# Optimization experiments

Measured on AMD Instinct MI355X. Metric: run time of the kernel, lower is better.

The kernel has to match this reference:

```python
import jax, jax.numpy as jnp
import numpy as np

D = 2048
H = 16
HD = D // H
EPS = 1e-5

def setup_inputs() -> dict:
    key = jax.random.key(0)
    ks = jax.random.split(key, 7)
    B, S = 4, 2048
    scale = 1.0 / np.sqrt(D)
    return {
        "hidden_states": jax.random.normal(ks[0], (B, S, D), dtype=jnp.float32),
        "ln_gamma": jnp.ones((D,), dtype=jnp.float32),
        "ln_beta": jnp.zeros((D,), dtype=jnp.float32),
        "W_qkv": jax.random.normal(ks[1], (D, 3 * D), dtype=jnp.float32) * scale,
        "b_qkv": jnp.zeros((3 * D,), dtype=jnp.float32),
        "W_proj": jax.random.normal(ks[2], (D, D), dtype=jnp.float32) * scale,
        "b_proj": jnp.zeros((D,), dtype=jnp.float32),
    }

def reference(hidden_states, ln_gamma, ln_beta, W_qkv, b_qkv, W_proj, b_proj):
    B, S, _ = hidden_states.shape
    # LayerNorm (fused into QKV projection in the original kernel)
    mu = jnp.mean(hidden_states, axis=-1, keepdims=True)
    var = jnp.mean(jnp.square(hidden_states - mu), axis=-1, keepdims=True)
    x = (hidden_states - mu) * jax.lax.rsqrt(var + EPS) * ln_gamma + ln_beta
    # QKV projection
    qkv = jnp.einsum("bsd,de->bse", x, W_qkv) + b_qkv  # [B,S,3D]
    q, k, v = jnp.split(qkv, 3, axis=-1)
    # split heads -> [B,H,S,hd]
    q = q.reshape(B, S, H, HD).transpose(0, 2, 1, 3)
    k = k.reshape(B, S, H, HD).transpose(0, 2, 1, 3)
    v = v.reshape(B, S, H, HD).transpose(0, 2, 1, 3)
    # scaled causal attention
    scores = jnp.einsum("bhqd,bhkd->bhqk", q, k) / jnp.asarray(np.sqrt(HD), q.dtype)
    causal = jnp.tril(jnp.ones((S, S), dtype=bool))
    neg = jnp.finfo(scores.dtype).min
    scores = jnp.where(causal, scores, neg)
    attn = jax.nn.softmax(scores, axis=-1)
    out = jnp.einsum("bhqk,bhkd->bhqd", attn, v)
    # merge heads, output projection (dropout is identity in eval / p=0)
    out = out.transpose(0, 2, 1, 3).reshape(B, S, D)
    return jnp.einsum("bsd,de->bse", out, W_proj) + b_proj
```

## Files before the change

### kernel.cpp

```cpp
#include <hip/hip_runtime.h>
#include <cstdint>

typedef __attribute__((ext_vector_type(8))) short bf16x8;
typedef __attribute__((ext_vector_type(4))) float f32x4;
typedef unsigned short u16;
typedef unsigned int u32;

constexpr int D   = 2048;
constexpr int H   = 16;
constexpr int HD  = 128;
constexpr int BATCH = 4;
constexpr int S   = 2048;
constexpr int ROWS = BATCH * S;
constexpr int N3D = 3 * D;
constexpr int QKW = 2 * D;

__device__ __forceinline__ u16 f2bf(float f) {
    union { float f; u32 u; } v; v.f = f;
    u32 r = v.u + 0x7FFFu + ((v.u >> 16) & 1u);
    return (u16)(r >> 16);
}

__device__ __forceinline__ void gld_lds16(const u16* g, u16* l) {
    __builtin_amdgcn_global_load_lds(
        (const __attribute__((address_space(1))) void*)g,
        (__attribute__((address_space(3))) void*)l, 16, 0, 0);
}

__global__ __launch_bounds__(256) void ln_bf16_kernel(
    const float* __restrict__ x, const float* __restrict__ gamma,
    const float* __restrict__ beta, u16* __restrict__ out)
{
    const int row = blockIdx.x;
    const int t = threadIdx.x;
    const float* xr = x + (size_t)row * D;
    float4 a = ((const float4*)xr)[2*t];
    float4 b = ((const float4*)xr)[2*t+1];
    float s  = a.x+a.y+a.z+a.w + b.x+b.y+b.z+b.w;
    float ss = a.x*a.x+a.y*a.y+a.z*a.z+a.w*a.w + b.x*b.x+b.y*b.y+b.z*b.z+b.w*b.w;
    #pragma unroll
    for (int off = 32; off > 0; off >>= 1) {
        s  += __shfl_down(s, off);
        ss += __shfl_down(ss, off);
    }
    __shared__ float red[8];
    const int wave = t >> 6, lane = t & 63;
    if (lane == 0) { red[wave] = s; red[4+wave] = ss; }
    __syncthreads();
    const float mu   = (red[0]+red[1]+red[2]+red[3]) * (1.0f/D);
    const float var  = (red[4]+red[5]+red[6]+red[7]) * (1.0f/D) - mu*mu;
    const float rstd = rsqrtf(var + 1e-5f);
    float4 g0  = ((const float4*)gamma)[2*t];
    float4 g1  = ((const float4*)gamma)[2*t+1];
    float4 be0 = ((const float4*)beta)[2*t];
    float4 be1 = ((const float4*)beta)[2*t+1];
    union { uint4 v; u16 e[8]; } o;
    o.e[0] = f2bf((a.x-mu)*rstd*g0.x + be0.x);
    o.e[1] = f2bf((a.y-mu)*rstd*g0.y + be0.y);
    o.e[2] = f2bf((a.z-mu)*rstd*g0.z + be0.z);
    o.e[3] = f2bf((a.w-mu)*rstd*g0.w + be0.w);
    o.e[4] = f2bf((b.x-mu)*rstd*g1.x + be1.x);
    o.e[5] = f2bf((b.y-mu)*rstd*g1.y + be1.y);
    o.e[6] = f2bf((b.z-mu)*rstd*g1.z + be1.z);
    o.e[7] = f2bf((b.w-mu)*rstd*g1.w + be1.w);
    ((uint4*)(out + (size_t)row*D))[t] = o.v;
}

__global__ __launch_bounds__(256) void transpose_bf16_kernel(
    const float* __restrict__ in, u16* __restrict__ out, int K, int N)
{
    __shared__ u16 tile[64][65];
    const int tn0 = blockIdx.x * 64;
    const int tk0 = blockIdx.y * 64;
    const int t = threadIdx.x;
    const int tx = t & 63;
    const int ty = t >> 6;
    #pragma unroll
    for (int i = 0; i < 16; i++) {
        int k = ty + i*4;
        tile[k][tx] = f2bf(in[(size_t)(tk0+k)*N + tn0 + tx]);
    }
    __syncthreads();
    #pragma unroll
    for (int i = 0; i < 16; i++) {
        int n = ty + i*4;
        out[(size_t)(tn0+n)*K + tk0 + tx] = tile[tx][n];
    }
}

constexpr int BM = 128, BN = 128, BK = 32;

template<int MODE>
__global__ __launch_bounds__(256) void gemm_bt_kernel(
    const u16* __restrict__ A, const u16* __restrict__ Bt,
    const float* __restrict__ bias, void* __restrict__ Cout,
    u16* __restrict__ vtb, int M, int N, int K)
{
    __shared__ u16 sA[BM * BK];
    __shared__ u16 sB[BN * BK];
    const int t = threadIdx.x;
    const int wave = t >> 6, lane = t & 63;
    const int lr = lane & 15, lq = lane >> 4;
    const int wm = (wave >> 1) * 64, wn = (wave & 1) * 64;
    const int m0 = blockIdx.y * BM, n0 = blockIdx.x * BN;

    const int srow = wave * 32 + (lane >> 2);
    const int scb  = (lane & 3) ^ ((lane >> 3) & 3);
    const int scol = scb * 8;
    u16* ldsA0 = sA + (wave*2 + 0) * 512;
    u16* ldsA1 = sA + (wave*2 + 1) * 512;
    u16* ldsB0 = sB + (wave*2 + 0) * 512;
    u16* ldsB1 = sB + (wave*2 + 1) * 512;
    const u16* gA0 = A  + (size_t)(m0 + srow     ) * K + scol;
    const u16* gA1 = A  + (size_t)(m0 + srow + 16) * K + scol;
    const u16* gB0 = Bt + (size_t)(n0 + srow     ) * K + scol;
    const u16* gB1 = Bt + (size_t)(n0 + srow + 16) * K + scol;

    const int rblk = (lq ^ ((lr >> 1) & 3)) * 8;

    f32x4 acc[4][4];
    #pragma unroll
    for (int i = 0; i < 4; i++)
        #pragma unroll
        for (int j = 0; j < 4; j++)
            acc[i][j] = (f32x4)(0.0f);

    for (int k0 = 0; k0 < K; k0 += BK) {
        __syncthreads();
        gld_lds16(gA0 + k0, ldsA0);
        gld_lds16(gA1 + k0, ldsA1);
        gld_lds16(gB0 + k0, ldsB0);
        gld_lds16(gB1 + k0, ldsB1);
        __syncthreads();
        bf16x8 af[4], bfr[4];
        #pragma unroll
        for (int mt = 0; mt < 4; mt++)
            af[mt] = *(const bf16x8*)(sA + (wm + mt*16 + lr) * BK + rblk);
        #pragma unroll
        for (int nt = 0; nt < 4; nt++)
            bfr[nt] = *(const bf16x8*)(sB + (wn + nt*16 + lr) * BK + rblk);
        #pragma unroll
        for (int mt = 0; mt < 4; mt++)
            #pragma unroll
            for (int nt = 0; nt < 4; nt++)
                acc[mt][nt] = __builtin_amdgcn_mfma_f32_16x16x32_bf16(
                    af[mt], bfr[nt], acc[mt][nt], 0, 0, 0);
    }

    #pragma unroll
    for (int mt = 0; mt < 4; mt++) {
        #pragma unroll
        for (int nt = 0; nt < 4; nt++) {
            const int col = n0 + wn + nt*16 + lr;
            const float bv = bias[col];
            const int row0 = m0 + wm + mt*16 + lq*4;
            float v[4];
            #pragma unroll
            for (int r = 0; r < 4; r++) v[r] = acc[mt][nt][r] + bv;
            if (MODE == 0) {
                #pragma unroll
                for (int r = 0; r < 4; r++)
                    ((float*)Cout)[(size_t)(row0 + r) * N + col] = v[r];
            } else {
                if (n0 < QKW) {
                    #pragma unroll
                    for (int r = 0; r < 4; r++)
                        ((u16*)Cout)[(size_t)(row0 + r) * QKW + col] = f2bf(v[r]);
                } else {
                    const int vcol = col - QKW;
                    const int b = row0 >> 11, s0 = row0 & 2047;
                    ushort4 pk;
                    pk.x = f2bf(v[0]); pk.y = f2bf(v[1]);
                    pk.z = f2bf(v[2]); pk.w = f2bf(v[3]);
                    *(ushort4*)(vtb + ((size_t)(b*H + (vcol >> 7)) * HD
                                       + (vcol & 127)) * S + s0) = pk;
                }
            }
        }
    }
}

constexpr int TQ = 64, TK = 64;
constexpr int KPAD = 136;
constexpr int VPAD = 72;
constexpr int PPAD = 72;

__global__ __launch_bounds__(256) void attn_kernel(
    const u16* __restrict__ qkb, const u16* __restrict__ vtb,
    u16* __restrict__ ctx)
{
    __shared__ u16 sK[TK * KPAD];
    __shared__ u16 sVT[HD * VPAD];
    __shared__ u16 sP[4 * 16 * PPAD];

    const int flat = blockIdx.x;
    const int qt = 31 - (flat >> 6);
    const int bh = flat & 63;
    const int b  = bh >> 4, h = bh & 15;
    const int q0 = qt * TQ;
    const int t = threadIdx.x;
    const int wave = t >> 6, lane = t & 63;
    const int lr = lane & 15, lq = lane >> 4;

    const u16* baseQK = qkb + (size_t)b * S * QKW + h * HD;
    const u16* baseVT = vtb + (size_t)bh * HD * S;

    const int qrow = q0 + wave * 16 + lr;
    bf16x8 qf[4];
    #pragma unroll
    for (int kc = 0; kc < 4; kc++)
        qf[kc] = *(const bf16x8*)(baseQK + (size_t)qrow * QKW + kc*32 + lq*8);

    float m_r[4], l_r[4];
    f32x4 o[8];
    #pragma unroll
    for (int r = 0; r < 4; r++) { m_r[r] = -1e30f; l_r[r] = 0.0f; }
    #pragma unroll
    for (int j = 0; j < 8; j++) o[j] = (f32x4)(0.0f);

    const float scale = 0.08838834764831845f;
    const int nkt = qt + 1;

    for (int kt = 0; kt < nkt; kt++) {
        __syncthreads();
        #pragma unroll
        for (int i = 0; i < 4; i++) {
            int c = t + i * 256;
            int krow = c >> 4, kcol = (c & 15) * 8;
            uint4 v = *(const uint4*)(baseQK + D + (size_t)(kt*TK + krow) * QKW + kcol);
            *(uint4*)(sK + krow * KPAD + kcol) = v;
        }
        #pragma unroll
        for (int i = 0; i < 4; i++) {
            int c = t + i * 256;
            int vrow = c >> 3, coff = (c & 7) * 8;
            uint4 v = *(const uint4*)(baseVT + (size_t)vrow * S + kt*TK + coff);
            *(uint4*)(sVT + vrow * VPAD + coff) = v;
        }
        __syncthreads();

        f32x4 sc[4];
        #pragma unroll
        for (int nt = 0; nt < 4; nt++) sc[nt] = (f32x4)(0.0f);
        #pragma unroll
        for (int nt = 0; nt < 4; nt++)
            #pragma unroll
            for (int kc = 0; kc < 4; kc++) {
                bf16x8 kf = *(const bf16x8*)(sK + (nt*16 + lr) * KPAD + kc*32 + lq*8);
                sc[nt] = __builtin_amdgcn_mfma_f32_16x16x32_bf16(qf[kc], kf, sc[nt], 0, 0, 0);
            }

        const bool diag = (kt == qt);
        float rowmax[4] = {-1e30f, -1e30f, -1e30f, -1e30f};
        const int qgb = q0 + wave*16 + lq*4;
        #pragma unroll
        for (int nt = 0; nt < 4; nt++)
            #pragma unroll
            for (int r = 0; r < 4; r++) {
                float sv = sc[nt][r] * scale;
                if (diag) {
                    const int kg = kt*TK + nt*16 + lr;
                    if (kg > qgb + r) sv = -1e30f;
                }
                sc[nt][r] = sv;
                rowmax[r] = fmaxf(rowmax[r], sv);
            }
        #pragma unroll
        for (int mask = 1; mask < 16; mask <<= 1)
            #pragma unroll
            for (int r = 0; r < 4; r++)
                rowmax[r] = fmaxf(rowmax[r], __shfl_xor(rowmax[r], mask));

        float alpha[4];
        #pragma unroll
        for (int r = 0; r < 4; r++) {
            float nm = fmaxf(m_r[r], rowmax[r]);
            alpha[r] = __expf(m_r[r] - nm);
            m_r[r] = nm;
        }

        u16* pw = sP + wave * 16 * PPAD;
        #pragma unroll
        for (int nt = 0; nt < 4; nt++) {
            #pragma unroll
            for (int r = 0; r < 4; r++) {
                float p = __expf(sc[nt][r] - m_r[r]);
                sc[nt][r] = p;
                pw[(lq*4 + r) * PPAD + nt*16 + lr] = f2bf(p);
            }
        }
        #pragma unroll
        for (int r = 0; r < 4; r++) {
            float psum = sc[0][r] + sc[1][r] + sc[2][r] + sc[3][r];
            l_r[r] = l_r[r] * alpha[r] + psum;
        }
        #pragma unroll
        for (int j = 0; j < 8; j++)
            #pragma unroll
            for (int r = 0; r < 4; r++)
                o[j][r] *= alpha[r];

        #pragma unroll
        for (int kc2 = 0; kc2 < 2; kc2++) {
            bf16x8 pa = *(const bf16x8*)(pw + lr * PPAD + kc2*32 + lq*8);
            #pragma unroll
            for (int n2 = 0; n2 < 8; n2++) {
                bf16x8 vb = *(const bf16x8*)(sVT + (n2*16 + lr) * VPAD + kc2*32 + lq*8);
                o[n2] = __builtin_amdgcn_mfma_f32_16x16x32_bf16(pa, vb, o[n2], 0, 0, 0);
            }
        }
    }

    #pragma unroll
    for (int mask = 1; mask < 16; mask <<= 1)
        #pragma unroll
        for (int r = 0; r < 4; r++)
            l_r[r] += __shfl_xor(l_r[r], mask);
    float inv_l[4];
    #pragma unroll
    for (int r = 0; r < 4; r++) inv_l[r] = 1.0f / l_r[r];
    #pragma unroll
    for (int n2 = 0; n2 < 8; n2++)
        #pragma unroll
        for (int r = 0; r < 4; r++) {
            const int qg = q0 + wave*16 + lq*4 + r;
            const float v = o[n2][r] * inv_l[r];
            ctx[(size_t)(b * S + qg) * D + h * HD + n2*16 + lr] = f2bf(v);
        }
}

extern "C" void kernel_launch(void* const* d_in, const int* in_sizes, int n_in,
                              void* d_out, int out_size, void* d_ws, size_t ws_size,
                              hipStream_t stream) {
    const float* hs    = (const float*)d_in[0];
    const float* gamma = (const float*)d_in[1];
    const float* beta  = (const float*)d_in[2];
    const float* Wqkv  = (const float*)d_in[3];
    const float* bqkv  = (const float*)d_in[4];
    const float* Wproj = (const float*)d_in[5];
    const float* bproj = (const float*)d_in[6];

    char* ws = (char*)d_ws;
    size_t off = 0;
    u16* xb   = (u16*)(ws + off); off += (size_t)ROWS * D * 2;
    u16* wtq  = (u16*)(ws + off); off += (size_t)N3D * D * 2;
    u16* wtp  = (u16*)(ws + off); off += (size_t)D * D * 2;
    u16* qkb  = (u16*)(ws + off); off += (size_t)ROWS * QKW * 2;
    u16* vtb  = (u16*)(ws + off); off += (size_t)ROWS * D * 2;
    u16* ctxb = (u16*)(ws + off);

    ln_bf16_kernel<<<ROWS, 256, 0, stream>>>(hs, gamma, beta, xb);
    transpose_bf16_kernel<<<dim3(N3D/64, D/64), 256, 0, stream>>>(Wqkv, wtq, D, N3D);
    transpose_bf16_kernel<<<dim3(D/64,   D/64), 256, 0, stream>>>(Wproj, wtp, D, D);
    gemm_bt_kernel<2><<<dim3(N3D/BN, ROWS/BM), 256, 0, stream>>>(
        xb, wtq, bqkv, qkb, vtb, ROWS, N3D, D);
    attn_kernel<<<dim3((S/TQ) * BATCH * H), 256, 0, stream>>>(qkb, vtb, ctxb);
    gemm_bt_kernel<0><<<dim3(D/BN, ROWS/BM), 256, 0, stream>>>(
        ctxb, wtp, bproj, (float*)d_out, nullptr, ROWS, D, D);
}
```

Before: 698.3 us.

## Use 256x256 GEMM tiles with 4-stage async LDS prefetch pipeline

Replaces the 128x128 single-buffered GEMM with a 256x256 tile, 512-thread kernel that keeps a 4-slot ring of LDS buffers filled by direct global-to-LDS loads issued three k-steps ahead. Waiting on partial vmcnt lets loads overlap the MFMA work, and setprio raises the wave's priority around the MFMA bursts. The LDS XOR swizzle is dropped, which may bring back bank conflicts. The larger tiles give fewer blocks, which may hurt occupancy and load balance, especially for the smaller output projection.

```diff
diff --git a/kernel.cpp b/kernel.cpp
--- a/kernel.cpp
+++ b/kernel.cpp
@@ -88,75 +88,101 @@
     }
 }
 
-constexpr int BM = 128, BN = 128, BK = 32;
+constexpr int BM = 256, BN = 256, BK = 32;
 
 template<int MODE>
-__global__ __launch_bounds__(256) void gemm_bt_kernel(
+__global__ __launch_bounds__(512, 2) void gemm256_kernel(
     const u16* __restrict__ A, const u16* __restrict__ Bt,
     const float* __restrict__ bias, void* __restrict__ Cout,
     u16* __restrict__ vtb, int M, int N, int K)
 {
-    __shared__ u16 sA[BM * BK];
-    __shared__ u16 sB[BN * BK];
+    __shared__ u16 sA[4 * 8192];
+    __shared__ u16 sB[4 * 8192];
+
     const int t = threadIdx.x;
     const int wave = t >> 6, lane = t & 63;
     const int lr = lane & 15, lq = lane >> 4;
-    const int wm = (wave >> 1) * 64, wn = (wave & 1) * 64;
+    const int wm = wave >> 2, wn = wave & 3;
     const int m0 = blockIdx.y * BM, n0 = blockIdx.x * BN;
 
-    const int srow = wave * 32 + (lane >> 2);
-    const int scb  = (lane & 3) ^ ((lane >> 3) & 3);
-    const int scol = scb * 8;
-    u16* ldsA0 = sA + (wave*2 + 0) * 512;
-    u16* ldsA1 = sA + (wave*2 + 1) * 512;
-    u16* ldsB0 = sB + (wave*2 + 0) * 512;
-    u16* ldsB1 = sB + (wave*2 + 1) * 512;
-    const u16* gA0 = A  + (size_t)(m0 + srow     ) * K + scol;
-    const u16* gA1 = A  + (size_t)(m0 + srow + 16) * K + scol;
-    const u16* gB0 = Bt + (size_t)(n0 + srow     ) * K + scol;
-    const u16* gB1 = Bt + (size_t)(n0 + srow + 16) * K + scol;
-
-    const int rblk = (lq ^ ((lr >> 1) & 3)) * 8;
-
-    f32x4 acc[4][4];
-    #pragma unroll
-    for (int i = 0; i < 4; i++)
+    const int g0 = t, g1 = t + 512;
+    const u16* gA0 = A  + (size_t)(m0 + (g0 >> 2)) * K + (g0 & 3) * 8;
+    const u16* gA1 = A  + (size_t)(m0 + (g1 >> 2)) * K + (g1 & 3) * 8;
+    const u16* gB0 = Bt + (size_t)(n0 + (g0 >> 2)) * K + (g0 & 3) * 8;
+    const u16* gB1 = Bt + (size_t)(n0 + (g1 >> 2)) * K + (g1 & 3) * 8;
+
+    f32x4 acc[8][4];
+    #pragma unroll
+    for (int i = 0; i < 8; i++)
         #pragma unroll
         for (int j = 0; j < 4; j++)
             acc[i][j] = (f32x4)(0.0f);
 
-    for (int k0 = 0; k0 < K; k0 += BK) {
-        __syncthreads();
-        gld_lds16(gA0 + k0, ldsA0);
-        gld_lds16(gA1 + k0, ldsA1);
-        gld_lds16(gB0 + k0, ldsB0);
-        gld_lds16(gB1 + k0, ldsB1);
-        __syncthreads();
-        bf16x8 af[4], bfr[4];
+    const int NT = K / BK;
+
+    auto STAGE = [&](int slot, int kt) {
+        u16* a = sA + slot * 8192 + wave * 512;
+        u16* b = sB + slot * 8192 + wave * 512;
+        const int ko = kt * BK;
+        gld_lds16(gA0 + ko, a);
+        gld_lds16(gA1 + ko, a + 4096);
+        gld_lds16(gB0 + ko, b);
+        gld_lds16(gB1 + ko, b + 4096);
+    };
+
+    STAGE(0, 0); STAGE(1, 1); STAGE(2, 2);
+
+    for (int kt = 0; kt < NT; ++kt) {
+        const int tp = (kt + 3 < NT) ? (kt + 3) : (NT - 1);
+        STAGE((kt + 3) & 3, tp);
+        asm volatile("s_waitcnt vmcnt(12)" ::: "memory");
+        __builtin_amdgcn_s_barrier();
+        __builtin_amdgcn_sched_barrier(0);
+
+        const u16* tAp = sA + (kt & 3) * 8192 + (wm * 128) * BK + lq * 8;
+        const u16* tBp = sB + (kt & 3) * 8192 + (wn * 64)  * BK + lq * 8;
+
+        bf16x8 bfr[4], af[4];
+        #pragma unroll
+        for (int nt = 0; nt < 4; nt++)
+            bfr[nt] = *(const bf16x8*)(tBp + (nt * 16 + lr) * BK);
         #pragma unroll
         for (int mt = 0; mt < 4; mt++)
-            af[mt] = *(const bf16x8*)(sA + (wm + mt*16 + lr) * BK + rblk);
-        #pragma unroll
-        for (int nt = 0; nt < 4; nt++)
-            bfr[nt] = *(const bf16x8*)(sB + (wn + nt*16 + lr) * BK + rblk);
+            af[mt] = *(const bf16x8*)(tAp + (mt * 16 + lr) * BK);
+        __builtin_amdgcn_s_setprio(1);
         #pragma unroll
         for (int mt = 0; mt < 4; mt++)
             #pragma unroll
             for (int nt = 0; nt < 4; nt++)
                 acc[mt][nt] = __builtin_amdgcn_mfma_f32_16x16x32_bf16(
                     af[mt], bfr[nt], acc[mt][nt], 0, 0, 0);
-    }
-
-    #pragma unroll
-    for (int mt = 0; mt < 4; mt++) {
+        __builtin_amdgcn_s_setprio(0);
+        #pragma unroll
+        for (int mt = 0; mt < 4; mt++)
+            af[mt] = *(const bf16x8*)(tAp + (64 + mt * 16 + lr) * BK);
+        __builtin_amdgcn_s_setprio(1);
+        #pragma unroll
+        for (int mt = 0; mt < 4; mt++)
+            #pragma unroll
+            for (int nt = 0; nt < 4; nt++)
+                acc[4 + mt][nt] = __builtin_amdgcn_mfma_f32_16x16x32_bf16(
+                    af[mt], bfr[nt], acc[4 + mt][nt], 0, 0, 0);
+        __builtin_amdgcn_s_setprio(0);
+        __builtin_amdgcn_sched_barrier(0);
+        __builtin_amdgcn_s_barrier();
+    }
+    asm volatile("s_waitcnt vmcnt(0)" ::: "memory");
+
+    #pragma unroll
+    for (int i = 0; i < 8; i++) {
+        const int row0 = m0 + wm * 128 + (i >> 2) * 64 + (i & 3) * 16 + lq * 4;
         #pragma unroll
         for (int nt = 0; nt < 4; nt++) {
-            const int col = n0 + wn + nt*16 + lr;
+            const int col = n0 + wn * 64 + nt * 16 + lr;
             const float bv = bias[col];
-            const int row0 = m0 + wm + mt*16 + lq*4;
             float v[4];
             #pragma unroll
-            for (int r = 0; r < 4; r++) v[r] = acc[mt][nt][r] + bv;
+            for (int r = 0; r < 4; r++) v[r] = acc[i][nt][r] + bv;
             if (MODE == 0) {
                 #pragma unroll
                 for (int r = 0; r < 4; r++)
@@ -352,9 +378,9 @@
     ln_bf16_kernel<<<ROWS, 256, 0, stream>>>(hs, gamma, beta, xb);
     transpose_bf16_kernel<<<dim3(N3D/64, D/64), 256, 0, stream>>>(Wqkv, wtq, D, N3D);
     transpose_bf16_kernel<<<dim3(D/64,   D/64), 256, 0, stream>>>(Wproj, wtp, D, D);
-    gemm_bt_kernel<2><<<dim3(N3D/BN, ROWS/BM), 256, 0, stream>>>(
+    gemm256_kernel<2><<<dim3(N3D/BN, ROWS/BM), 512, 0, stream>>>(
         xb, wtq, bqkv, qkb, vtb, ROWS, N3D, D);
     attn_kernel<<<dim3((S/TQ) * BATCH * H), 256, 0, stream>>>(qkb, vtb, ctxb);
-    gemm_bt_kernel<0><<<dim3(D/BN, ROWS/BM), 256, 0, stream>>>(
+    gemm256_kernel<0><<<dim3(D/BN, ROWS/BM), 512, 0, stream>>>(
         ctxb, wtp, bproj, (float*)d_out, nullptr, ROWS, D, D);
 }
```

Result: faster. 682.3 us (-2.3%).
